# Kernel optimization log

Measured on AMD Instinct MI355X. Metric: run time of the kernel, lower is better.

Reference implementation:

```python
import jax, jax.numpy as jnp
import numpy as np

V = 512          # num vertices
F = 64           # pair-feature dim (gpnn_channels in)
C = 64           # gpnn_channels out
E = 8192         # num edges (avg degree 16)


def setup_inputs() -> dict:
    key = jax.random.key(0)
    k1, k2, k3, k4 = jax.random.split(key, 4)
    alpha = jax.random.normal(k1, (V * V, F), dtype=jnp.float32)          # pair features, row v*V+w
    edge_index = jax.random.randint(k2, (2, E), 0, V)                      # COO [src; dst]
    # GPNNEdgeConv.nn = MLP([F, C, C], act='relu')  (norm treated as identity / eval stats)
    w1 = jax.random.normal(k3, (F, C), dtype=jnp.float32) * (1.0 / np.sqrt(F))
    b1 = jnp.zeros((C,), dtype=jnp.float32)
    w2 = jax.random.normal(k4, (C, C), dtype=jnp.float32) * (1.0 / np.sqrt(C))
    b2 = jnp.zeros((C,), dtype=jnp.float32)
    eps = jnp.asarray(0.0, dtype=jnp.float32)                              # train_eps parameter
    return {"alpha": alpha, "edge_index": edge_index,
            "w1": w1, "b1": b1, "w2": w2, "b2": b2, "eps": eps}


def reference(alpha, edge_index, w1, b1, w2, b2, eps):
    # Dense 0/1 adjacency adj_t: adj[v, j] = 1 iff edge j -> v (dst-indexed, as spmm(adj_t, .)).
    adj = jnp.zeros((V, V), dtype=alpha.dtype).at[edge_index[1], edge_index[0]].set(1.0)
    a3 = alpha.reshape(V, V, F)  # a3[v, j] = alpha[v*V + j]
    # message_and_aggregate: out[v*V+w] = row v of spmm(adj_t, A_{v,w}),
    # where A_{v,w}[j] = alpha[v*V+j] + alpha[w*V+j]  (sum aggregation)
    #   = sum_j adj[v,j] * (a3[v,j] + a3[w,j]) = S[v] + T[v,w]
    S = jnp.einsum('vj,vjf->vf', adj, a3)    # [V, F]
    T = jnp.einsum('vj,wjf->vwf', adj, a3)   # [V, V, F]
    out = (S[:, None, :] + T).reshape(V * V, F)
    # GINConv residual: out + (1 + eps) * x_r, then MLP (Linear-ReLU-Linear)
    out = out + (1.0 + eps) * alpha
    h = jax.nn.relu(out @ w1 + b1)
    return h @ w2 + b2
```

## Files before the change

### kernel.cpp

```cpp
#include <hip/hip_runtime.h>
#include <hip/hip_bf16.h>

#define NV 512
#define NF 64

typedef __attribute__((ext_vector_type(8))) short bf16x8;
typedef __attribute__((ext_vector_type(4))) float f32x4;

union BF8 { bf16x8 v; unsigned u[4]; };

__device__ __forceinline__ unsigned short f2bf(float x) {
    unsigned u = __float_as_uint(x);
    unsigned r = (u + 0x7fffu + ((u >> 16) & 1u)) >> 16;
    return (unsigned short)r;
}

__device__ __forceinline__ unsigned awt_addr(int f, int jbyte) {
    return (unsigned)((f * 1024 + jbyte) ^ (((f ^ (f >> 3)) & 7) << 4));
}
__device__ __forceinline__ unsigned wt_addr(int m, int n, int kbyte) {
    return (unsigned)(m * 8192 + ((n * 128 + kbyte) ^ (((n ^ (n >> 3)) & 7) << 4)));
}

__global__ void k_zero(unsigned int* mask) {
    mask[blockIdx.x * 256 + threadIdx.x] = 0u;
}

__global__ void k_edges(const int* __restrict__ ei, int E, unsigned int* __restrict__ mask) {
    int e = blockIdx.x * 256 + threadIdx.x;
    if (e < E) {
        int s = ei[e];
        int d = ei[E + e];
        atomicOr(&mask[d * 16 + (s >> 5)], 1u << (s & 31));
    }
}

__global__ void k_S(const unsigned int* __restrict__ mask, const float* __restrict__ alpha,
                    float* __restrict__ S) {
    __shared__ float red[4][64];
    int v = blockIdx.x;
    int lane = threadIdx.x & 63;
    int g = threadIdx.x >> 6;
    float a0 = 0.f, a1 = 0.f;
    for (int wd = g * 4; wd < g * 4 + 4; ++wd) {
        unsigned bits = mask[v * 16 + wd];
        while (bits) {
            int b0 = __ffs(bits) - 1; bits &= bits - 1;
            float x0 = alpha[((size_t)v * NV + wd * 32 + b0) * NF + lane];
            if (bits) {
                int b1 = __ffs(bits) - 1; bits &= bits - 1;
                a1 += alpha[((size_t)v * NV + wd * 32 + b1) * NF + lane];
            }
            a0 += x0;
        }
    }
    red[g][lane] = a0 + a1;
    __syncthreads();
    if (g == 0)
        S[v * NF + lane] = red[0][lane] + red[1][lane] + red[2][lane] + red[3][lane];
}

#define SCR_OFF 65536

__global__ __launch_bounds__(512, 4) void k_main(
    const float* __restrict__ alpha, const float* __restrict__ w1, const float* __restrict__ b1,
    const float* __restrict__ w2, const float* __restrict__ b2, const float* __restrict__ eps_p,
    const unsigned int* __restrict__ mask, const float* __restrict__ S,
    float* __restrict__ out)
{
    extern __shared__ char smem[];

    const int w    = blockIdx.x;
    const int t    = threadIdx.x;
    const int lane = t & 63;
    const int wid  = t >> 6;
    const int nlo  = lane & 15;
    const int g    = lane >> 4;
    const int mbase = wid * 64;
    const float* src = alpha + (size_t)w * (NV * NF);

    auto stage_half = [&](int i) {
        int task = i * 512 + t;
        int jb = task >> 4;
        int fq = task & 15;
        unsigned ua[4][4];
#pragma unroll
        for (int h = 0; h < 4; ++h) {
            f32x4 r0 = *(const f32x4*)(src + (size_t)(jb * 8 + 2 * h) * NF + fq * 4);
            f32x4 r1 = *(const f32x4*)(src + (size_t)(jb * 8 + 2 * h + 1) * NF + fq * 4);
#pragma unroll
            for (int c = 0; c < 4; ++c)
                ua[c][h] = (unsigned)f2bf(r0[c]) | ((unsigned)f2bf(r1[c]) << 16);
        }
#pragma unroll
        for (int c = 0; c < 4; ++c) {
            BF8 p;
            p.u[0] = ua[c][0]; p.u[1] = ua[c][1]; p.u[2] = ua[c][2]; p.u[3] = ua[c][3];
            *(bf16x8*)(smem + awt_addr(fq * 4 + c, jb * 16)) = p.v;
        }
    };

    f32x4 acc[4][4];
#pragma unroll
    for (int mi = 0; mi < 4; ++mi)
#pragma unroll
        for (int nt = 0; nt < 4; ++nt)
            acc[mi][nt] = (f32x4){0.f, 0.f, 0.f, 0.f};

    const unsigned int* maskrow = mask + (size_t)(mbase + nlo) * 16;

    auto gemm8 = [&](int K0) {
#pragma unroll 2
        for (int kx = 0; kx < 8; ++kx) {
            const int kk = K0 + kx;
            unsigned wv[4];
#pragma unroll
            for (int mi = 0; mi < 4; ++mi) wv[mi] = maskrow[mi * 256 + kk];
            BF8 afr[4];
#pragma unroll
            for (int mi = 0; mi < 4; ++mi) {
                unsigned byteb = (wv[mi] >> (g * 8)) & 0xFFu;
#pragma unroll
                for (int h = 0; h < 4; ++h) {
                    unsigned b0 = (byteb >> (2 * h)) & 1u;
                    unsigned b1 = (byteb >> (2 * h + 1)) & 1u;
                    afr[mi].u[h] = (b0 ? 0x3F80u : 0u) | (b1 ? 0x3F800000u : 0u);
                }
            }
#pragma unroll
            for (int nt = 0; nt < 4; ++nt) {
                bf16x8 bfr = *(const bf16x8*)(smem + awt_addr(nt * 16 + nlo, kk * 64 + g * 16));
#pragma unroll
                for (int mi = 0; mi < 4; ++mi)
                    acc[mi][nt] = __builtin_amdgcn_mfma_f32_16x16x32_bf16(afr[mi].v, bfr, acc[mi][nt], 0, 0, 0);
            }
        }
    };

    stage_half(0);
    __syncthreads();
    stage_half(1);
    gemm8(0);
    __syncthreads();
    gemm8(8);
    __syncthreads();

    if (t < 256) {
        int m  = t >> 7;
        int sub = t & 127;
        int jb = sub >> 4;
        int fq = sub & 15;
        const float* wsrc = m ? w2 : w1;
        unsigned ua[4][4];
#pragma unroll
        for (int h = 0; h < 4; ++h) {
            f32x4 r0 = *(const f32x4*)(wsrc + (size_t)(jb * 8 + 2 * h) * NF + fq * 4);
            f32x4 r1 = *(const f32x4*)(wsrc + (size_t)(jb * 8 + 2 * h + 1) * NF + fq * 4);
#pragma unroll
            for (int c = 0; c < 4; ++c)
                ua[c][h] = (unsigned)f2bf(r0[c]) | ((unsigned)f2bf(r1[c]) << 16);
        }
#pragma unroll
        for (int c = 0; c < 4; ++c) {
            BF8 p;
            p.u[0] = ua[c][0]; p.u[1] = ua[c][1]; p.u[2] = ua[c][2]; p.u[3] = ua[c][3];
            *(bf16x8*)(smem + wt_addr(m, fq * 4 + c, jb * 16)) = p.v;
        }
    }
    float b1v[4], b2v[4];
#pragma unroll
    for (int nt = 0; nt < 4; ++nt) {
        b1v[nt] = b1[nt * 16 + nlo];
        b2v[nt] = b2[nt * 16 + nlo];
    }
    const float ceps = 1.0f + eps_p[0];

    __syncthreads();

    char* myscr = smem + SCR_OFF + wid * 2048;
#pragma unroll
    for (int mi = 0; mi < 4; ++mi) {
        int v0 = mbase + mi * 16;
#pragma unroll
        for (int nt = 0; nt < 4; ++nt) {
            int f = nt * 16 + nlo;
#pragma unroll
            for (int r = 0; r < 4; ++r) {
                int v = v0 + g * 4 + r;
                float pre = acc[mi][nt][r] + S[v * NF + f]
                          + ceps * alpha[((size_t)v * NV + w) * NF + f];
                int row = g * 4 + r;
                *(unsigned short*)(myscr + row * 128 + ((2 * f) ^ ((row & 7) << 4))) = f2bf(pre);
            }
        }

        bf16x8 a0 = *(const bf16x8*)(myscr + nlo * 128 + ((g * 16) ^ ((nlo & 7) << 4)));
        bf16x8 a1 = *(const bf16x8*)(myscr + nlo * 128 + ((g * 16 + 64) ^ ((nlo & 7) << 4)));
        f32x4 accm[4];
#pragma unroll
        for (int nt = 0; nt < 4; ++nt) {
            bf16x8 wf0 = *(const bf16x8*)(smem + wt_addr(0, nt * 16 + nlo, g * 16));
            bf16x8 wf1 = *(const bf16x8*)(smem + wt_addr(0, nt * 16 + nlo, 64 + g * 16));
            f32x4 z = {0.f, 0.f, 0.f, 0.f};
            z = __builtin_amdgcn_mfma_f32_16x16x32_bf16(a0, wf0, z, 0, 0, 0);
            z = __builtin_amdgcn_mfma_f32_16x16x32_bf16(a1, wf1, z, 0, 0, 0);
            accm[nt] = z;
        }

#pragma unroll
        for (int nt = 0; nt < 4; ++nt)
#pragma unroll
            for (int r = 0; r < 4; ++r) {
                float hv = accm[nt][r] + b1v[nt];
                hv = hv > 0.f ? hv : 0.f;
                int row = g * 4 + r;
                *(unsigned short*)(myscr + row * 128 + ((2 * (nt * 16 + nlo)) ^ ((row & 7) << 4))) = f2bf(hv);
            }

        bf16x8 h0 = *(const bf16x8*)(myscr + nlo * 128 + ((g * 16) ^ ((nlo & 7) << 4)));
        bf16x8 h1 = *(const bf16x8*)(myscr + nlo * 128 + ((g * 16 + 64) ^ ((nlo & 7) << 4)));
#pragma unroll
        for (int nt = 0; nt < 4; ++nt) {
            bf16x8 wf0 = *(const bf16x8*)(smem + wt_addr(1, nt * 16 + nlo, g * 16));
            bf16x8 wf1 = *(const bf16x8*)(smem + wt_addr(1, nt * 16 + nlo, 64 + g * 16));
            f32x4 z = {0.f, 0.f, 0.f, 0.f};
            z = __builtin_amdgcn_mfma_f32_16x16x32_bf16(h0, wf0, z, 0, 0, 0);
            z = __builtin_amdgcn_mfma_f32_16x16x32_bf16(h1, wf1, z, 0, 0, 0);
#pragma unroll
            for (int r = 0; r < 4; ++r) {
                int vv = v0 + g * 4 + r;
                out[((size_t)vv * NV + w) * NF + nt * 16 + nlo] = z[r] + b2v[nt];
            }
        }
    }
}

extern "C" void kernel_launch(void* const* d_in, const int* in_sizes, int n_in,
                              void* d_out, int out_size, void* d_ws, size_t ws_size,
                              hipStream_t stream) {
    const float* alpha = (const float*)d_in[0];
    const int*   ei    = (const int*)d_in[1];
    const float* w1    = (const float*)d_in[2];
    const float* b1    = (const float*)d_in[3];
    const float* w2    = (const float*)d_in[4];
    const float* b2    = (const float*)d_in[5];
    const float* eps   = (const float*)d_in[6];
    float* out = (float*)d_out;
    int E = in_sizes[1] / 2;

    unsigned int* mask = (unsigned int*)d_ws;
    float* S = (float*)d_ws + 8192;

    k_zero <<<32, 256, 0, stream>>>(mask);
    k_edges<<<(E + 255) / 256, 256, 0, stream>>>(ei, E, mask);
    k_S    <<<NV, 256, 0, stream>>>(mask, alpha, S);

    const int smem_bytes = 81920;
    hipFuncSetAttribute(reinterpret_cast<const void*>(k_main),
                        hipFuncAttributeMaxDynamicSharedMemorySize, smem_bytes);
    k_main <<<NV, 512, smem_bytes, stream>>>(alpha, w1, b1, w2, b2, eps, mask, S, out);
}
```

Measured before the change: 71.35 us.

## Vectorize mask loads, seed accumulators with S, batch alpha loads, nontemporal stores

The mask words are now loaded four at a time as uint4 instead of one scalar load per k-step, and the accumulators start from S rather than adding S in the epilogue. In the epilogue all sixteen alpha values for a row tile are loaded up front so the loads can overlap. Output writes use nontemporal stores to avoid polluting cache, and the zeroing kernel is replaced with hipMemsetAsync. These are several small memory-access tweaks aimed at the bandwidth-bound output path, at the cost of more registers held live.

```diff
diff --git a/kernel.cpp b/kernel.cpp
--- a/kernel.cpp
+++ b/kernel.cpp
@@ -20,10 +20,6 @@
 }
 __device__ __forceinline__ unsigned wt_addr(int m, int n, int kbyte) {
     return (unsigned)(m * 8192 + ((n * 128 + kbyte) ^ (((n ^ (n >> 3)) & 7) << 4)));
-}
-
-__global__ void k_zero(unsigned int* mask) {
-    mask[blockIdx.x * 256 + threadIdx.x] = 0u;
 }
 
 __global__ void k_edges(const int* __restrict__ ei, int E, unsigned int* __restrict__ mask) {
@@ -101,25 +97,33 @@
     };
 
     f32x4 acc[4][4];
+
+    stage_half(0);
+
 #pragma unroll
     for (int mi = 0; mi < 4; ++mi)
 #pragma unroll
         for (int nt = 0; nt < 4; ++nt)
-            acc[mi][nt] = (f32x4){0.f, 0.f, 0.f, 0.f};
-
-    const unsigned int* maskrow = mask + (size_t)(mbase + nlo) * 16;
-
-    auto gemm8 = [&](int K0) {
-#pragma unroll 2
-        for (int kx = 0; kx < 8; ++kx) {
-            const int kk = K0 + kx;
-            unsigned wv[4];
-#pragma unroll
-            for (int mi = 0; mi < 4; ++mi) wv[mi] = maskrow[mi * 256 + kk];
+#pragma unroll
+            for (int r = 0; r < 4; ++r)
+                acc[mi][nt][r] = S[(size_t)(mbase + mi * 16 + g * 4 + r) * NF + nt * 16 + nlo];
+
+    __syncthreads();
+
+    auto gemm_q = [&](int kq) {
+        unsigned qw[4][4];
+#pragma unroll
+        for (int mi = 0; mi < 4; ++mi) {
+            const uint4 q = *(const uint4*)(mask + (size_t)(mbase + mi * 16 + nlo) * 16 + kq * 4);
+            qw[mi][0] = q.x; qw[mi][1] = q.y; qw[mi][2] = q.z; qw[mi][3] = q.w;
+        }
+#pragma unroll
+        for (int kr = 0; kr < 4; ++kr) {
+            const int kk = kq * 4 + kr;
             BF8 afr[4];
 #pragma unroll
             for (int mi = 0; mi < 4; ++mi) {
-                unsigned byteb = (wv[mi] >> (g * 8)) & 0xFFu;
+                unsigned byteb = (qw[mi][kr] >> (g * 8)) & 0xFFu;
 #pragma unroll
                 for (int h = 0; h < 4; ++h) {
                     unsigned b0 = (byteb >> (2 * h)) & 1u;
@@ -137,12 +141,12 @@
         }
     };
 
-    stage_half(0);
-    __syncthreads();
     stage_half(1);
-    gemm8(0);
-    __syncthreads();
-    gemm8(8);
+    gemm_q(0);
+    gemm_q(1);
+    __syncthreads();
+    gemm_q(2);
+    gemm_q(3);
     __syncthreads();
 
     if (t < 256) {
@@ -181,14 +185,20 @@
 #pragma unroll
     for (int mi = 0; mi < 4; ++mi) {
         int v0 = mbase + mi * 16;
+
+        float rvv[4][4];
+#pragma unroll
+        for (int nt = 0; nt < 4; ++nt)
+#pragma unroll
+            for (int r = 0; r < 4; ++r)
+                rvv[nt][r] = alpha[((size_t)(v0 + g * 4 + r) * NV + w) * NF + nt * 16 + nlo];
+
 #pragma unroll
         for (int nt = 0; nt < 4; ++nt) {
             int f = nt * 16 + nlo;
 #pragma unroll
             for (int r = 0; r < 4; ++r) {
-                int v = v0 + g * 4 + r;
-                float pre = acc[mi][nt][r] + S[v * NF + f]
-                          + ceps * alpha[((size_t)v * NV + w) * NF + f];
+                float pre = acc[mi][nt][r] + ceps * rvv[nt][r];
                 int row = g * 4 + r;
                 *(unsigned short*)(myscr + row * 128 + ((2 * f) ^ ((row & 7) << 4))) = f2bf(pre);
             }
@@ -229,7 +239,8 @@
 #pragma unroll
             for (int r = 0; r < 4; ++r) {
                 int vv = v0 + g * 4 + r;
-                out[((size_t)vv * NV + w) * NF + nt * 16 + nlo] = z[r] + b2v[nt];
+                __builtin_nontemporal_store(z[r] + b2v[nt],
+                    out + ((size_t)vv * NV + w) * NF + nt * 16 + nlo);
             }
         }
     }
@@ -251,7 +262,7 @@
     unsigned int* mask = (unsigned int*)d_ws;
     float* S = (float*)d_ws + 8192;
 
-    k_zero <<<32, 256, 0, stream>>>(mask);
+    hipMemsetAsync(mask, 0, 8192 * sizeof(unsigned int), stream);
     k_edges<<<(E + 255) / 256, 256, 0, stream>>>(ei, E, mask);
     k_S    <<<NV, 256, 0, stream>>>(mask, alpha, S);
 
```

Measured after the change: 73.20 us. 1.03x slower.
